# Optimization experiments

Measured on AMD Instinct MI355X. Metric: run time of the kernel, lower is better.

Reference implementation:

```python
import jax, jax.numpy as jnp
import numpy as np

B, T, DIM, NH = 4, 2048, 1024, 16
HD = DIM // NH


def setup_inputs() -> dict:
    key = jax.random.key(0)
    ks = jax.random.split(key, 9)
    s = 0.02
    return {
        "x": jax.random.normal(ks[0], (B, T, DIM), dtype=jnp.float32),
        "Wq": jax.random.normal(ks[1], (DIM, DIM), dtype=jnp.float32) * s,
        "bq": jnp.zeros((DIM,), dtype=jnp.float32),
        "Wk": jax.random.normal(ks[2], (DIM, DIM), dtype=jnp.float32) * s,
        "bk": jnp.zeros((DIM,), dtype=jnp.float32),
        "Wv": jax.random.normal(ks[3], (DIM, DIM), dtype=jnp.float32) * s,
        "bv": jnp.zeros((DIM,), dtype=jnp.float32),
        "Wo": jax.random.normal(ks[4], (DIM, DIM), dtype=jnp.float32) * s,
        "bo": jnp.zeros((DIM,), dtype=jnp.float32),
    }


def reference(x, Wq, bq, Wk, bk, Wv, bv, Wo, bo):
    scale = HD ** -0.5
    # QKV projections (torch Linear: x @ W.T + b; here W stored as [in, out])
    q = (x @ Wq + bq).reshape(B, T, NH, HD).transpose(0, 2, 1, 3)  # [B,H,T,D]
    k = (x @ Wk + bk).reshape(B, T, NH, HD).transpose(0, 2, 1, 3)
    v = (x @ Wv + bv).reshape(B, T, NH, HD).transpose(0, 2, 1, 3)
    scores = jnp.einsum("bhqd,bhkd->bhqk", q, k) * scale  # [B,H,T,T]
    attn = jax.nn.softmax(scores, axis=-1)
    out = jnp.einsum("bhqk,bhkd->bhqd", attn, v)  # [B,H,T,D]
    out = out.transpose(0, 2, 1, 3).reshape(B, T, DIM)
    return out @ Wo + bo
```

## Files before the change

### kernel.cpp

```cpp
#include <hip/hip_runtime.h>
#include <math.h>

#define BB   4
#define TT   2048
#define DIMM 1024
#define NHH  16
#define HDD  64
#define MM   (BB * TT)

typedef unsigned short u16;
typedef unsigned int   u32;
typedef short bf16x8 __attribute__((ext_vector_type(8)));
typedef float f32x4  __attribute__((ext_vector_type(4)));

__device__ __forceinline__ u16 f2bf(float f) {
    u32 u = __float_as_uint(f);
    return (u16)((u + 0x7fffu + ((u >> 16) & 1u)) >> 16);
}

__device__ __forceinline__ f32x4 mfma16(bf16x8 a, bf16x8 b, f32x4 c) {
    return __builtin_amdgcn_mfma_f32_16x16x32_bf16(a, b, c, 0, 0, 0);
}

__device__ __forceinline__ float exp2_raw(float x) {
    float r;
    asm("v_exp_f32 %0, %1" : "=v"(r) : "v"(x));
    return r;
}

__device__ __forceinline__ int swz8(int row, int slot) {
    return ((slot ^ (row & 7) ^ ((row >> 3) & 7)) & 7) * 8;
}
__device__ __forceinline__ int swz4(int row, int slot) {
    return ((slot ^ (row & 3)) & 3) * 8;
}

__global__ void prep_w_x(const float* __restrict__ W0,
                         const float* __restrict__ W1,
                         const float* __restrict__ W2,
                         const float* __restrict__ W3,
                         u16* __restrict__ T0, u16* __restrict__ T1,
                         u16* __restrict__ T2, u16* __restrict__ T3,
                         const float* __restrict__ x, u16* __restrict__ xb) {
    __shared__ float tile[32][33];
    const int z   = blockIdx.z;
    const int tid = threadIdx.x;
    if (z == 4) {
        const int bid = blockIdx.y * 32 + blockIdx.x;
#pragma unroll
        for (int c = 0; c < 4; ++c) {
            int i = ((bid * 4 + c) * 256 + tid) * 8;
            float4 a = *(const float4*)(x + i);
            float4 b = *(const float4*)(x + i + 4);
            u32 w0 = f2bf(a.x) | ((u32)f2bf(a.y) << 16);
            u32 w1 = f2bf(a.z) | ((u32)f2bf(a.w) << 16);
            u32 w2 = f2bf(b.x) | ((u32)f2bf(b.y) << 16);
            u32 w3 = f2bf(b.z) | ((u32)f2bf(b.w) << 16);
            *(uint4*)(xb + i) = make_uint4(w0, w1, w2, w3);
        }
        return;
    }
    const float* W = (z == 0) ? W0 : (z == 1) ? W1 : (z == 2) ? W2 : W3;
    u16*        Wt = (z == 0) ? T0 : (z == 1) ? T1 : (z == 2) ? T2 : T3;
    const int c  = tid & 31;
    const int r8 = tid >> 5;
    const int kb = blockIdx.y * 32, nb = blockIdx.x * 32;
#pragma unroll
    for (int rr = 0; rr < 4; ++rr) {
        int r = r8 + rr * 8;
        tile[r][c] = W[(kb + r) * 1024 + nb + c];
    }
    __syncthreads();
#pragma unroll
    for (int rr = 0; rr < 4; ++rr) {
        int r = r8 + rr * 8;
        Wt[(nb + r) * 1024 + kb + c] = f2bf(tile[c][r]);
    }
}

__global__ __launch_bounds__(256, 2) void gemm_qkv(
    const u16* __restrict__ A, const u16* __restrict__ Bt,
    const float* __restrict__ bq, const float* __restrict__ bk,
    const float* __restrict__ bv,
    u16* __restrict__ Qout, u16* __restrict__ Kout, u16* __restrict__ Vout,
    float qscale)
{
    __shared__ u16 As[128 * 32];
    __shared__ u16 Bs[128 * 32];

    const int tid  = threadIdx.x;
    const int m0   = blockIdx.x * 128;
    const int n0   = blockIdx.y * 128;
    const int wave = tid >> 6, lane = tid & 63;
    const int wr = wave >> 1, wc = wave & 1;
    const int l15 = lane & 15, l4 = lane >> 4;

    const int r0 = tid >> 2, ks = tid & 3;
    const int r1 = r0 + 64;
    const int w0 = r0 * 32 + swz4(r0, ks);
    const int w1 = r1 * 32 + swz4(r1, ks);

    f32x4 acc[4][4];
#pragma unroll
    for (int i = 0; i < 4; ++i)
#pragma unroll
        for (int j = 0; j < 4; ++j) acc[i][j] = (f32x4){0.f, 0.f, 0.f, 0.f};

    const u16* Ar0 = A  + (m0 + r0) * 1024 + ks * 8;
    const u16* Ar1 = A  + (m0 + r1) * 1024 + ks * 8;
    const u16* Br0 = Bt + (n0 + r0) * 1024 + ks * 8;
    const u16* Br1 = Bt + (n0 + r1) * 1024 + ks * 8;

    uint4 a0 = *(const uint4*)Ar0;
    uint4 a1 = *(const uint4*)Ar1;
    uint4 b0 = *(const uint4*)Br0;
    uint4 b1 = *(const uint4*)Br1;
    *(uint4*)&As[w0] = a0; *(uint4*)&As[w1] = a1;
    *(uint4*)&Bs[w0] = b0; *(uint4*)&Bs[w1] = b1;
    __syncthreads();

    for (int kt = 0; kt < 32; ++kt) {
        if (kt < 31) {
            const int ko = (kt + 1) * 32;
            a0 = *(const uint4*)(Ar0 + ko);
            a1 = *(const uint4*)(Ar1 + ko);
            b0 = *(const uint4*)(Br0 + ko);
            b1 = *(const uint4*)(Br1 + ko);
        }
        bf16x8 af[4], bf[4];
#pragma unroll
        for (int rt = 0; rt < 4; ++rt) {
            int row = wr * 64 + rt * 16 + l15;
            af[rt] = *(const bf16x8*)&As[row * 32 + swz4(row, l4)];
            int col = wc * 64 + rt * 16 + l15;
            bf[rt] = *(const bf16x8*)&Bs[col * 32 + swz4(col, l4)];
        }
#pragma unroll
        for (int rt = 0; rt < 4; ++rt)
#pragma unroll
            for (int ct = 0; ct < 4; ++ct)
                acc[rt][ct] = mfma16(af[rt], bf[ct], acc[rt][ct]);
        __syncthreads();
        if (kt < 31) {
            *(uint4*)&As[w0] = a0; *(uint4*)&As[w1] = a1;
            *(uint4*)&Bs[w0] = b0; *(uint4*)&Bs[w1] = b1;
            __syncthreads();
        }
    }

    const int mode = n0 >> 10;
    const float* bias = (mode == 0) ? bq : (mode == 1) ? bk : bv;
    const float osc = (mode == 0) ? qscale : 1.0f;
    u16* Sout = (mode == 0) ? Qout : Kout;

#pragma unroll
    for (int rt = 0; rt < 4; ++rt)
#pragma unroll
        for (int ct = 0; ct < 4; ++ct) {
            int n  = n0 + wc * 64 + ct * 16 + l15;
            int nn = n & 1023;
            float bn = bias[nn];
            int h = nn >> 6, d = nn & 63;
            if (mode == 2) {
                int m00 = m0 + wr * 64 + rt * 16 + l4 * 4;
                int b = m00 >> 11, t0 = m00 & 2047;
                ushort4 pk;
                pk.x = f2bf(acc[rt][ct][0] + bn);
                pk.y = f2bf(acc[rt][ct][1] + bn);
                pk.z = f2bf(acc[rt][ct][2] + bn);
                pk.w = f2bf(acc[rt][ct][3] + bn);
                *(ushort4*)(&Vout[((((b << 4) + h) * 64 + d) << 11) + t0]) = pk;
            } else {
#pragma unroll
                for (int i = 0; i < 4; ++i) {
                    int m = m0 + wr * 64 + rt * 16 + l4 * 4 + i;
                    int b = m >> 11, t = m & 2047;
                    Sout[(((b << 4) + h) * 2048 + t) * 64 + d] =
                        f2bf((acc[rt][ct][i] + bn) * osc);
                }
            }
        }
}

__global__ __launch_bounds__(256, 2) void gemm_out(
    const u16* __restrict__ A, const u16* __restrict__ Bt,
    const float* __restrict__ bias, float* __restrict__ Cout)
{
    __shared__ u16 As[128 * 32];
    __shared__ u16 Bs[128 * 32];

    const int tid  = threadIdx.x;
    const int m0   = blockIdx.x * 128;
    const int n0   = blockIdx.y * 128;
    const int wave = tid >> 6, lane = tid & 63;
    const int wr = wave >> 1, wc = wave & 1;
    const int l15 = lane & 15, l4 = lane >> 4;

    const int r0 = tid >> 2, ks = tid & 3;
    const int r1 = r0 + 64;
    const int w0 = r0 * 32 + swz4(r0, ks);
    const int w1 = r1 * 32 + swz4(r1, ks);

    f32x4 acc[4][4];
#pragma unroll
    for (int i = 0; i < 4; ++i)
#pragma unroll
        for (int j = 0; j < 4; ++j) acc[i][j] = (f32x4){0.f, 0.f, 0.f, 0.f};

    const u16* Ar0 = A  + (m0 + r0) * 1024 + ks * 8;
    const u16* Ar1 = A  + (m0 + r1) * 1024 + ks * 8;
    const u16* Br0 = Bt + (n0 + r0) * 1024 + ks * 8;
    const u16* Br1 = Bt + (n0 + r1) * 1024 + ks * 8;

    uint4 a0 = *(const uint4*)Ar0;
    uint4 a1 = *(const uint4*)Ar1;
    uint4 b0 = *(const uint4*)Br0;
    uint4 b1 = *(const uint4*)Br1;
    *(uint4*)&As[w0] = a0; *(uint4*)&As[w1] = a1;
    *(uint4*)&Bs[w0] = b0; *(uint4*)&Bs[w1] = b1;
    __syncthreads();

    for (int kt = 0; kt < 32; ++kt) {
        if (kt < 31) {
            const int ko = (kt + 1) * 32;
            a0 = *(const uint4*)(Ar0 + ko);
            a1 = *(const uint4*)(Ar1 + ko);
            b0 = *(const uint4*)(Br0 + ko);
            b1 = *(const uint4*)(Br1 + ko);
        }
        bf16x8 af[4], bf[4];
#pragma unroll
        for (int rt = 0; rt < 4; ++rt) {
            int row = wr * 64 + rt * 16 + l15;
            af[rt] = *(const bf16x8*)&As[row * 32 + swz4(row, l4)];
            int col = wc * 64 + rt * 16 + l15;
            bf[rt] = *(const bf16x8*)&Bs[col * 32 + swz4(col, l4)];
        }
#pragma unroll
        for (int rt = 0; rt < 4; ++rt)
#pragma unroll
            for (int ct = 0; ct < 4; ++ct)
                acc[rt][ct] = mfma16(af[rt], bf[ct], acc[rt][ct]);
        __syncthreads();
        if (kt < 31) {
            *(uint4*)&As[w0] = a0; *(uint4*)&As[w1] = a1;
            *(uint4*)&Bs[w0] = b0; *(uint4*)&Bs[w1] = b1;
            __syncthreads();
        }
    }

#pragma unroll
    for (int rt = 0; rt < 4; ++rt)
#pragma unroll
        for (int ct = 0; ct < 4; ++ct) {
            int n = n0 + wc * 64 + ct * 16 + l15;
            float bn = bias[n];
#pragma unroll
            for (int i = 0; i < 4; ++i) {
                int m = m0 + wr * 64 + rt * 16 + l4 * 4 + i;
                Cout[m * 1024 + n] = acc[rt][ct][i] + bn;
            }
        }
}

__global__ __launch_bounds__(256, 4) void attn_mfma(
    const u16* __restrict__ Qb, const u16* __restrict__ Kb,
    const u16* __restrict__ Vtg, u16* __restrict__ Ob)
{
    __shared__ u16 Ks[2][64 * 64];
    __shared__ u16 Vts[2][64 * 64];
    __shared__ u16 Ps[4][16 * 64];

    const int tid   = threadIdx.x;
    const int g     = blockIdx.x;
    const int chunk = (g & 7) * 256 + (g >> 3);
    const int bh    = chunk >> 5;
    const int q0    = (chunk & 31) * 64;
    const int b     = bh >> 4, h = bh & 15;
    const u16* Qp   = Qb + (bh * TT + q0) * HDD;
    const u16* Kp   = Kb + bh * TT * HDD;
    const u16* Vp   = Vtg + bh * TT * HDD;

    const int wave = tid >> 6, lane = tid & 63;
    const int l15 = lane & 15, l4 = lane >> 4;

    bf16x8 qf[2];
#pragma unroll
    for (int hf = 0; hf < 2; ++hf)
        qf[hf] = *(const bf16x8*)(Qp + (wave * 16 + l15) * HDD + hf * 32 + l4 * 8);

    f32x4 oacc[4];
    float mr = -INFINITY, lr = 0.f;
#pragma unroll
    for (int db = 0; db < 4; ++db) oacc[db] = (f32x4){0.f, 0.f, 0.f, 0.f};

    const int pxor = (l15 & 7) ^ ((l15 >> 3) << 2);
    u32* const Pw = (u32*)&Ps[wave][0];
    int pidx[8];
#pragma unroll
    for (int nt = 0; nt < 4; ++nt)
#pragma unroll
        for (int pp = 0; pp < 2; ++pp) {
            int k2 = nt * 16 + l4 * 4 + 2 * pp;
            int slotW = ((k2 >> 3) ^ pxor) & 7;
            pidx[nt * 2 + pp] = (l15 * 64 + slotW * 8 + (k2 & 7)) >> 1;
        }
    int pread[2];
#pragma unroll
    for (int hf = 0; hf < 2; ++hf)
        pread[hf] = l15 * 64 + ((((hf << 2) + l4) ^ pxor) & 7) * 8;

    const int r0 = tid >> 3, ds = tid & 7;
    const int r1 = r0 + 32;
    const int wo0 = r0 * 64 + swz8(r0, ds);
    const int wo1 = r1 * 64 + swz8(r1, ds);

    uint4 kr0, kr1, vr0, vr1;
    kr0 = *(const uint4*)(Kp + r0 * 64 + ds * 8);
    kr1 = *(const uint4*)(Kp + r1 * 64 + ds * 8);
    vr0 = *(const uint4*)(Vp + r0 * 2048 + ds * 8);
    vr1 = *(const uint4*)(Vp + r1 * 2048 + ds * 8);
    *(uint4*)&Ks[0][wo0]  = kr0;
    *(uint4*)&Ks[0][wo1]  = kr1;
    *(uint4*)&Vts[0][wo0] = vr0;
    *(uint4*)&Vts[0][wo1] = vr1;
    __syncthreads();

    for (int kv = 0; kv < TT / 64; ++kv) {
        const int cur = kv & 1;

        if (kv < TT / 64 - 1) {
            const u16* Kt = Kp + (kv + 1) * 64 * HDD;
            const u16* Vt = Vp + (kv + 1) * 64;
            kr0 = *(const uint4*)(Kt + r0 * 64 + ds * 8);
            kr1 = *(const uint4*)(Kt + r1 * 64 + ds * 8);
            vr0 = *(const uint4*)(Vt + r0 * 2048 + ds * 8);
            vr1 = *(const uint4*)(Vt + r1 * 2048 + ds * 8);
        }

        f32x4 sacc[4];
#pragma unroll
        for (int nt = 0; nt < 4; ++nt) sacc[nt] = (f32x4){0.f, 0.f, 0.f, 0.f};
        __builtin_amdgcn_s_setprio(1);
#pragma unroll
        for (int nt = 0; nt < 4; ++nt) {
            int krow = nt * 16 + l15;
#pragma unroll
            for (int hf = 0; hf < 2; ++hf) {
                bf16x8 kf = *(const bf16x8*)&Ks[cur][krow * 64 + swz8(krow, hf * 4 + l4)];
                sacc[nt] = mfma16(kf, qf[hf], sacc[nt]);
            }
        }
        __builtin_amdgcn_s_setprio(0);

        auto pack_pass = [&]() -> float {
            float ls0 = 0.f, ls1 = 0.f;
#pragma unroll
            for (int nt = 0; nt < 4; ++nt)
#pragma unroll
                for (int pp = 0; pp < 2; ++pp) {
                    float pa = exp2_raw(sacc[nt][2 * pp]     - mr);
                    float pb = exp2_raw(sacc[nt][2 * pp + 1] - mr);
                    ls0 += pa; ls1 += pb;
                    u32 pk;
                    asm("v_cvt_pk_bf16_f32 %0, %1, %2" : "=v"(pk) : "v"(pa), "v"(pb));
                    Pw[pidx[nt * 2 + pp]] = pk;
                }
            return ls0 + ls1;
        };
        float lsum = pack_pass();
        if (__builtin_expect(__any(!(lsum < 1e30f)), 0)) {
            float mx = sacc[0][0];
#pragma unroll
            for (int nt = 0; nt < 4; ++nt)
#pragma unroll
                for (int i = 0; i < 4; ++i) mx = fmaxf(mx, sacc[nt][i]);
            mx = fmaxf(mx, __shfl_xor(mx, 16, 64));
            mx = fmaxf(mx, __shfl_xor(mx, 32, 64));
            float mnew = fmaxf(mr, mx);
            float rsc  = (mr == -INFINITY) ? 0.f : exp2_raw(mr - mnew);
            mr = mnew;
            lr *= rsc;
            float rr[4];
#pragma unroll
            for (int i = 0; i < 4; ++i) rr[i] = __shfl(rsc, l4 * 4 + i, 16);
#pragma unroll
            for (int db = 0; db < 4; ++db)
#pragma unroll
                for (int i = 0; i < 4; ++i) oacc[db][i] *= rr[i];
            lsum = pack_pass();
        }
        lr += lsum;

        bf16x8 pf[2];
#pragma unroll
        for (int hf = 0; hf < 2; ++hf)
            pf[hf] = *(const bf16x8*)&Ps[wave][pread[hf]];
        __builtin_amdgcn_s_setprio(1);
#pragma unroll
        for (int db = 0; db < 4; ++db) {
            int d = db * 16 + l15;
#pragma unroll
            for (int hf = 0; hf < 2; ++hf) {
                bf16x8 vf = *(const bf16x8*)&Vts[cur][d * 64 + swz8(d, hf * 4 + l4)];
                oacc[db] = mfma16(pf[hf], vf, oacc[db]);
            }
        }
        __builtin_amdgcn_s_setprio(0);

        if (kv < TT / 64 - 1) {
            const int nxt = cur ^ 1;
            *(uint4*)&Ks[nxt][wo0]  = kr0;
            *(uint4*)&Ks[nxt][wo1]  = kr1;
            *(uint4*)&Vts[nxt][wo0] = vr0;
            *(uint4*)&Vts[nxt][wo1] = vr1;
        }
        __syncthreads();
    }

    lr += __shfl_xor(lr, 16, 64);
    lr += __shfl_xor(lr, 32, 64);
    float inv[4];
#pragma unroll
    for (int i = 0; i < 4; ++i) inv[i] = 1.f / __shfl(lr, l4 * 4 + i, 16);
#pragma unroll
    for (int db = 0; db < 4; ++db)
#pragma unroll
        for (int i = 0; i < 4; ++i) {
            int t   = q0 + wave * 16 + l4 * 4 + i;
            int col = h * 64 + db * 16 + l15;
            Ob[(b * TT + t) * DIMM + col] = f2bf(oacc[db][i] * inv[i]);
        }
}

extern "C" void kernel_launch(void* const* d_in, const int* in_sizes, int n_in,
                              void* d_out, int out_size, void* d_ws, size_t ws_size,
                              hipStream_t stream)
{
    const float* x  = (const float*)d_in[0];
    const float* Wq = (const float*)d_in[1];
    const float* bq = (const float*)d_in[2];
    const float* Wk = (const float*)d_in[3];
    const float* bk = (const float*)d_in[4];
    const float* Wv = (const float*)d_in[5];
    const float* bv = (const float*)d_in[6];
    const float* Wo = (const float*)d_in[7];
    const float* bo = (const float*)d_in[8];

    u16* xb   = (u16*)d_ws;
    u16* wcat = xb   + 8388608;
    u16* wot  = wcat + 3145728;
    u16* qbuf = wot  + 1048576;
    u16* obuf = qbuf + 8388608;
    u16* kbuf = (u16*)d_out;
    u16* vbuf = kbuf + 8388608;

    prep_w_x<<<dim3(32, 32, 5), 256, 0, stream>>>(
        Wq, Wk, Wv, Wo, wcat, wcat + 1048576, wcat + 2097152, wot, x, xb);

    const float qscale = 0.125f * 1.44269504f;
    gemm_qkv<<<dim3(MM / 128, 3 * DIMM / 128), 256, 0, stream>>>(
        xb, wcat, bq, bk, bv, qbuf, kbuf, vbuf, qscale);

    attn_mfma<<<BB * NHH * (TT / 64), 256, 0, stream>>>(qbuf, kbuf, vbuf, obuf);

    gemm_out<<<dim3(MM / 128, DIMM / 128), 256, 0, stream>>>(obuf, wot, bo,
                                                             (float*)d_out);
}
```

Baseline: 221.1 us.

## Process two 64-row query sub-tiles per attention block to reuse K/V tiles

Each attention workgroup now handles 128 query rows instead of 64, with each wave holding two sets of Q fragments, accumulators and softmax state. Every K/V tile loaded into shared memory is reused for both sub-tiles, halving global K/V traffic and barrier count per query row. The grid is halved and register pressure roughly doubles for accumulators, which may reduce occupancy under the 4-block launch bound or cause spills. The per-wave P buffer is reused sequentially across the two sub-tiles.

Measured after the change: 327.6 us. +48.1%, slower.

```diff
diff --git a/kernel.cpp b/kernel.cpp
--- a/kernel.cpp
+++ b/kernel.cpp
@@ -273,9 +273,9 @@
 
     const int tid   = threadIdx.x;
     const int g     = blockIdx.x;
-    const int chunk = (g & 7) * 256 + (g >> 3);
-    const int bh    = chunk >> 5;
-    const int q0    = (chunk & 31) * 64;
+    const int chunk = (g & 7) * 128 + (g >> 3);
+    const int bh    = chunk >> 4;
+    const int q0    = (chunk & 15) * 128;
     const int b     = bh >> 4, h = bh & 15;
     const u16* Qp   = Qb + (bh * TT + q0) * HDD;
     const u16* Kp   = Kb + bh * TT * HDD;
@@ -284,15 +284,21 @@
     const int wave = tid >> 6, lane = tid & 63;
     const int l15 = lane & 15, l4 = lane >> 4;
 
-    bf16x8 qf[2];
-#pragma unroll
-    for (int hf = 0; hf < 2; ++hf)
-        qf[hf] = *(const bf16x8*)(Qp + (wave * 16 + l15) * HDD + hf * 32 + l4 * 8);
-
-    f32x4 oacc[4];
-    float mr = -INFINITY, lr = 0.f;
-#pragma unroll
-    for (int db = 0; db < 4; ++db) oacc[db] = (f32x4){0.f, 0.f, 0.f, 0.f};
+    bf16x8 qf[2][2];
+#pragma unroll
+    for (int qs = 0; qs < 2; ++qs)
+#pragma unroll
+        for (int hf = 0; hf < 2; ++hf)
+            qf[qs][hf] = *(const bf16x8*)(Qp + (qs * 64 + wave * 16 + l15) * HDD
+                                          + hf * 32 + l4 * 8);
+
+    f32x4 oacc[2][4];
+    float mr[2] = {-INFINITY, -INFINITY};
+    float lr[2] = {0.f, 0.f};
+#pragma unroll
+    for (int qs = 0; qs < 2; ++qs)
+#pragma unroll
+        for (int db = 0; db < 4; ++db) oacc[qs][db] = (f32x4){0.f, 0.f, 0.f, 0.f};
 
     const int pxor = (l15 & 7) ^ ((l15 >> 3) << 2);
     u32* const Pw = (u32*)&Ps[wave][0];
@@ -338,9 +344,11 @@
             vr1 = *(const uint4*)(Vt + r1 * 2048 + ds * 8);
         }
 
-        f32x4 sacc[4];
-#pragma unroll
-        for (int nt = 0; nt < 4; ++nt) sacc[nt] = (f32x4){0.f, 0.f, 0.f, 0.f};
+        f32x4 sacc[2][4];
+#pragma unroll
+        for (int qs = 0; qs < 2; ++qs)
+#pragma unroll
+            for (int nt = 0; nt < 4; ++nt) sacc[qs][nt] = (f32x4){0.f, 0.f, 0.f, 0.f};
         __builtin_amdgcn_s_setprio(1);
 #pragma unroll
         for (int nt = 0; nt < 4; ++nt) {
@@ -348,65 +356,69 @@
 #pragma unroll
             for (int hf = 0; hf < 2; ++hf) {
                 bf16x8 kf = *(const bf16x8*)&Ks[cur][krow * 64 + swz8(krow, hf * 4 + l4)];
-                sacc[nt] = mfma16(kf, qf[hf], sacc[nt]);
+                sacc[0][nt] = mfma16(kf, qf[0][hf], sacc[0][nt]);
+                sacc[1][nt] = mfma16(kf, qf[1][hf], sacc[1][nt]);
             }
         }
         __builtin_amdgcn_s_setprio(0);
 
-        auto pack_pass = [&]() -> float {
-            float ls0 = 0.f, ls1 = 0.f;
-#pragma unroll
-            for (int nt = 0; nt < 4; ++nt)
-#pragma unroll
-                for (int pp = 0; pp < 2; ++pp) {
-                    float pa = exp2_raw(sacc[nt][2 * pp]     - mr);
-                    float pb = exp2_raw(sacc[nt][2 * pp + 1] - mr);
-                    ls0 += pa; ls1 += pb;
-                    u32 pk;
-                    asm("v_cvt_pk_bf16_f32 %0, %1, %2" : "=v"(pk) : "v"(pa), "v"(pb));
-                    Pw[pidx[nt * 2 + pp]] = pk;
+#pragma unroll
+        for (int qs = 0; qs < 2; ++qs) {
+            auto pack_pass = [&]() -> float {
+                float ls0 = 0.f, ls1 = 0.f;
+#pragma unroll
+                for (int nt = 0; nt < 4; ++nt)
+#pragma unroll
+                    for (int pp = 0; pp < 2; ++pp) {
+                        float pa = exp2_raw(sacc[qs][nt][2 * pp]     - mr[qs]);
+                        float pb = exp2_raw(sacc[qs][nt][2 * pp + 1] - mr[qs]);
+                        ls0 += pa; ls1 += pb;
+                        u32 pk;
+                        asm("v_cvt_pk_bf16_f32 %0, %1, %2" : "=v"(pk) : "v"(pa), "v"(pb));
+                        Pw[pidx[nt * 2 + pp]] = pk;
+                    }
+                return ls0 + ls1;
+            };
+            float lsum = pack_pass();
+            if (__builtin_expect(__any(!(lsum < 1e30f)), 0)) {
+                float mx = sacc[qs][0][0];
+#pragma unroll
+                for (int nt = 0; nt < 4; ++nt)
+#pragma unroll
+                    for (int i = 0; i < 4; ++i) mx = fmaxf(mx, sacc[qs][nt][i]);
+                mx = fmaxf(mx, __shfl_xor(mx, 16, 64));
+                mx = fmaxf(mx, __shfl_xor(mx, 32, 64));
+                float mnew = fmaxf(mr[qs], mx);
+                float rsc  = (mr[qs] == -INFINITY) ? 0.f : exp2_raw(mr[qs] - mnew);
+                mr[qs] = mnew;
+                lr[qs] *= rsc;
+                float rr[4];
+#pragma unroll
+                for (int i = 0; i < 4; ++i) rr[i] = __shfl(rsc, l4 * 4 + i, 16);
+#pragma unroll
+                for (int db = 0; db < 4; ++db)
+#pragma unroll
+                    for (int i = 0; i < 4; ++i) oacc[qs][db][i] *= rr[i];
+                lsum = pack_pass();
+            }
+            lr[qs] += lsum;
+
+            bf16x8 pf[2];
+#pragma unroll
+            for (int hf = 0; hf < 2; ++hf)
+                pf[hf] = *(const bf16x8*)&Ps[wave][pread[hf]];
+            __builtin_amdgcn_s_setprio(1);
+#pragma unroll
+            for (int db = 0; db < 4; ++db) {
+                int d = db * 16 + l15;
+#pragma unroll
+                for (int hf = 0; hf < 2; ++hf) {
+                    bf16x8 vf = *(const bf16x8*)&Vts[cur][d * 64 + swz8(d, hf * 4 + l4)];
+                    oacc[qs][db] = mfma16(pf[hf], vf, oacc[qs][db]);
                 }
-            return ls0 + ls1;
-        };
-        float lsum = pack_pass();
-        if (__builtin_expect(__any(!(lsum < 1e30f)), 0)) {
-            float mx = sacc[0][0];
-#pragma unroll
-            for (int nt = 0; nt < 4; ++nt)
-#pragma unroll
-                for (int i = 0; i < 4; ++i) mx = fmaxf(mx, sacc[nt][i]);
-            mx = fmaxf(mx, __shfl_xor(mx, 16, 64));
-            mx = fmaxf(mx, __shfl_xor(mx, 32, 64));
-            float mnew = fmaxf(mr, mx);
-            float rsc  = (mr == -INFINITY) ? 0.f : exp2_raw(mr - mnew);
-            mr = mnew;
-            lr *= rsc;
-            float rr[4];
-#pragma unroll
-            for (int i = 0; i < 4; ++i) rr[i] = __shfl(rsc, l4 * 4 + i, 16);
-#pragma unroll
-            for (int db = 0; db < 4; ++db)
-#pragma unroll
-                for (int i = 0; i < 4; ++i) oacc[db][i] *= rr[i];
-            lsum = pack_pass();
-        }
-        lr += lsum;
-
-        bf16x8 pf[2];
-#pragma unroll
-        for (int hf = 0; hf < 2; ++hf)
-            pf[hf] = *(const bf16x8*)&Ps[wave][pread[hf]];
-        __builtin_amdgcn_s_setprio(1);
-#pragma unroll
-        for (int db = 0; db < 4; ++db) {
-            int d = db * 16 + l15;
-#pragma unroll
-            for (int hf = 0; hf < 2; ++hf) {
-                bf16x8 vf = *(const bf16x8*)&Vts[cur][d * 64 + swz8(d, hf * 4 + l4)];
-                oacc[db] = mfma16(pf[hf], vf, oacc[db]);
-            }
-        }
-        __builtin_amdgcn_s_setprio(0);
+            }
+            __builtin_amdgcn_s_setprio(0);
+        }
 
         if (kv < TT / 64 - 1) {
             const int nxt = cur ^ 1;
@@ -418,19 +430,23 @@
         __syncthreads();
     }
 
-    lr += __shfl_xor(lr, 16, 64);
-    lr += __shfl_xor(lr, 32, 64);
-    float inv[4];
-#pragma unroll
-    for (int i = 0; i < 4; ++i) inv[i] = 1.f / __shfl(lr, l4 * 4 + i, 16);
-#pragma unroll
-    for (int db = 0; db < 4; ++db)
-#pragma unroll
-        for (int i = 0; i < 4; ++i) {
-            int t   = q0 + wave * 16 + l4 * 4 + i;
-            int col = h * 64 + db * 16 + l15;
-            Ob[(b * TT + t) * DIMM + col] = f2bf(oacc[db][i] * inv[i]);
-        }
+#pragma unroll
+    for (int qs = 0; qs < 2; ++qs) {
+        float lrq = lr[qs];
+        lrq += __shfl_xor(lrq, 16, 64);
+        lrq += __shfl_xor(lrq, 32, 64);
+        float inv[4];
+#pragma unroll
+        for (int i = 0; i < 4; ++i) inv[i] = 1.f / __shfl(lrq, l4 * 4 + i, 16);
+#pragma unroll
+        for (int db = 0; db < 4; ++db)
+#pragma unroll
+            for (int i = 0; i < 4; ++i) {
+                int t   = q0 + qs * 64 + wave * 16 + l4 * 4 + i;
+                int col = h * 64 + db * 16 + l15;
+                Ob[(b * TT + t) * DIMM + col] = f2bf(oacc[qs][db][i] * inv[i]);
+            }
+    }
 }
 
 extern "C" void kernel_launch(void* const* d_in, const int* in_sizes, int n_in,
@@ -462,7 +478,7 @@
     gemm_qkv<<<dim3(MM / 128, 3 * DIMM / 128), 256, 0, stream>>>(
         xb, wcat, bq, bk, bv, qbuf, kbuf, vbuf, qscale);
 
-    attn_mfma<<<BB * NHH * (TT / 64), 256, 0, stream>>>(qbuf, kbuf, vbuf, obuf);
+    attn_mfma<<<BB * NHH * (TT / 128), 256, 0, stream>>>(qbuf, kbuf, vbuf, obuf);
 
     gemm_out<<<dim3(MM / 128, DIMM / 128), 256, 0, stream>>>(obuf, wot, bo,
                                                              (float*)d_out);
```
